# Kernel optimization log

Hardware: AMD Instinct MI355X
Metric: run time of the kernel (lower is better)

The kernel has to match this reference:

```python
import jax, jax.numpy as jnp
import numpy as np

NUM_BINS = 4
SCALE = 5.0
EPS = 1e-12

def hswish(x):
    return x * jnp.clip(x + 3.0, 0.0, 6.0) / 6.0

def l2norm(x, axis):
    n = jnp.sqrt(jnp.sum(x * x, axis=axis, keepdims=True))
    return x / jnp.maximum(n, EPS)

def setup_inputs() -> dict:
    key = jax.random.key(0)
    k0, k1, k2, k3, k4 = jax.random.split(key, 5)
    B, C, T, H, W = 8, 256, 32, 28, 28
    hidden, embd = 512, 32
    x = jax.random.normal(k0, (B, C, T, H, W), dtype=jnp.float32)
    W1 = jax.random.normal(k1, (hidden, C), dtype=jnp.float32) * (1.0 / np.sqrt(C))
    b1 = jax.random.normal(k2, (hidden,), dtype=jnp.float32) * 0.01
    W2 = jax.random.normal(k3, (embd, hidden), dtype=jnp.float32) * (1.0 / np.sqrt(hidden))
    b2 = jax.random.normal(k4, (embd,), dtype=jnp.float32) * 0.01
    return {"x": x, "W1": W1, "b1": b1, "W2": W2, "b2": b2}

def reference(x, W1, b1, W2, b2):
    B, C, T, H, W = x.shape
    # encoder: global spatial avg-pool -> 1x1x1 conv -> HSwish -> 1x1x1 conv
    pooled = jnp.mean(x, axis=(3, 4))                      # (B,C,T)
    h = hswish(jnp.einsum('hc,bct->bht', W1, pooled) + b1[None, :, None])
    embds = jnp.einsum('eh,bht->bet', W2, h) + b2[None, :, None]   # (B,E,T)
    norm_embd = l2norm(embds, axis=1)

    # --- grouping (no-grad in original) ---
    ns = jnp.sum(norm_embd[:, :, 1:] * norm_embd[:, :, :-1], axis=1)    # (B,T-1)
    # k-th smallest neighbour similarity = threshold
    smallest = -jax.lax.top_k(-ns, NUM_BINS - 1)[0]                      # ascending smallest k
    threshold = smallest[:, -1]
    edges = (ns > threshold[:, None]).astype(jnp.int32)                  # (B,T-1)
    interval_ends = jnp.concatenate(
        [jnp.zeros((B, 1), dtype=jnp.int32), 1 - edges], axis=1)        # (B,T)
    groups = jnp.cumsum(interval_ends, axis=1)                           # (B,T)
    group_ids = jnp.arange(NUM_BINS, dtype=groups.dtype)
    group_mask = (groups[:, :, None] == group_ids[None, None, :]).astype(jnp.float32)  # (B,T,K)
    group_sizes = jnp.sum(group_mask, axis=1, keepdims=True)             # (B,1,K)
    centers_sum = jnp.einsum('bet,btk->bek', norm_embd, group_mask)      # (B,E,K)
    norm_centers = l2norm(centers_sum / group_sizes, axis=1)             # (B,E,K)
    norm_centers = jax.lax.stop_gradient(norm_centers)

    similarities = jnp.einsum('bet,bek->btk', norm_embd, norm_centers)   # (B,T,K)
    weights = jax.nn.softmax(SCALE * similarities, axis=2)               # (B,T,K)
    sum_weights = jnp.sum(weights, axis=1, keepdims=True)                # (B,1,K)
    scales = jnp.where(sum_weights > 0.0, 1.0 / sum_weights, jnp.ones_like(sum_weights))
    scales = jax.lax.stop_gradient(scales)
    norm_weights = scales * weights                                      # (B,T,K)

    # weighted temporal pooling: avoids (B,C,T,K,H,W) blowup
    out = jnp.einsum('bcthw,btk->bckhw', x, norm_weights)                # (B,C,K,H,W)
    return out
```

## Files before the change

### kernel.cpp

```cpp
#include <hip/hip_runtime.h>
#include <math.h>

#define BATCH 8
#define CCH   256
#define TT    32
#define HWSZ  784
#define HID   512
#define EMB   32
#define KBINS 4
#define SCALEF 5.0f
#define EPSN  1e-12f

__global__ void pool_kernel(const float* __restrict__ x, float* __restrict__ pooled) {
    const int wave = threadIdx.x >> 6;
    const int lane = threadIdx.x & 63;
    const int row  = blockIdx.x * 4 + wave;
    const float4* xp = (const float4*)(x + (size_t)row * HWSZ);
    float s = 0.f;
    for (int f = lane; f < 196; f += 64) {
        float4 v = xp[f];
        s += v.x + v.y + v.z + v.w;
    }
#pragma unroll
    for (int off = 32; off > 0; off >>= 1) s += __shfl_down(s, off);
    if (lane == 0) pooled[row] = s * (1.0f / 784.0f);
}

__global__ void fc1_kernel(const float* __restrict__ W1, const float* __restrict__ b1,
                           const float* __restrict__ pooled, float* __restrict__ h) {
    const int b   = blockIdx.x >> 6;
    const int seg = blockIdx.x & 63;
    const int t   = threadIdx.x & 31;
    const int hid = seg * 8 + (threadIdx.x >> 5);
    const float* pb = pooled + (size_t)b * CCH * TT + t;
    const float* w  = W1 + (size_t)hid * CCH;
    float acc = 0.f;
#pragma unroll 8
    for (int c = 0; c < CCH; c++) acc += w[c] * pb[c * TT];
    acc += b1[hid];
    float r = fminf(fmaxf(acc + 3.0f, 0.0f), 6.0f);
    h[((size_t)b * HID + hid) * TT + t] = acc * r * (1.0f / 6.0f);
}

__global__ void fc2_kernel(const float* __restrict__ W2, const float* __restrict__ b2,
                           const float* __restrict__ h, float* __restrict__ embds) {
    const int o = blockIdx.x * 256 + threadIdx.x;
    const int b = o >> 10;
    const int e = (o >> 5) & 31;
    const int t = o & 31;
    const float* w  = W2 + (size_t)e * HID;
    const float* hp = h + (size_t)b * HID * TT + t;
    float acc = 0.f;
#pragma unroll 8
    for (int hd = 0; hd < HID; hd++) acc += w[hd] * hp[hd * TT];
    embds[o] = acc + b2[e];
}

__global__ void group_kernel(const float* __restrict__ embds, float* __restrict__ nw) {
    __shared__ float se[EMB][TT + 1];
    __shared__ float ns[TT];
    __shared__ float tmpns[TT];
    __shared__ float colinv[TT];
    __shared__ float cs[EMB][KBINS];
    __shared__ float wts[TT][KBINS];
    __shared__ float gsize[KBINS];
    __shared__ float kfac[KBINS];
    __shared__ int   gid[TT];

    const int b   = blockIdx.x;
    const int tid = threadIdx.x;

    for (int i = tid; i < EMB * TT; i += 256) {
        se[i >> 5][i & 31] = embds[(size_t)b * EMB * TT + i];
    }
    __syncthreads();

    if (tid < TT) {
        float s = 0.f;
        for (int e = 0; e < EMB; e++) { float v = se[e][tid]; s += v * v; }
        colinv[tid] = 1.0f / fmaxf(sqrtf(s), EPSN);
    }
    __syncthreads();
    for (int i = tid; i < EMB * TT; i += 256) {
        int e = i >> 5, t = i & 31;
        se[e][t] *= colinv[t];
    }
    __syncthreads();

    if (tid < TT - 1) {
        float s = 0.f;
        for (int e = 0; e < EMB; e++) s += se[e][tid] * se[e][tid + 1];
        ns[tid] = s;
    }
    __syncthreads();

    if (tid == 0) {
        for (int i = 0; i < TT - 1; i++) tmpns[i] = ns[i];
        float thr = 0.f;
        for (int p = 0; p < KBINS - 1; p++) {
            int jm = 0; float m = tmpns[0];
            for (int i = 1; i < TT - 1; i++) if (tmpns[i] < m) { m = tmpns[i]; jm = i; }
            thr = m;
            tmpns[jm] = __builtin_inff();
        }
        int g = 0; gid[0] = 0;
        for (int t = 1; t < TT; t++) { if (!(ns[t - 1] > thr)) g++; gid[t] = g; }
        for (int k = 0; k < KBINS; k++) {
            float c = 0.f;
            for (int t = 0; t < TT; t++) if (gid[t] == k) c += 1.0f;
            gsize[k] = c;
        }
    }
    __syncthreads();

    if (tid < EMB * KBINS) {
        int e = tid >> 2, k = tid & 3;
        float s = 0.f;
        for (int t = 0; t < TT; t++) if (gid[t] == k) s += se[e][t];
        cs[e][k] = s / gsize[k];
    }
    __syncthreads();
    if (tid < KBINS) {
        float s = 0.f;
        for (int e = 0; e < EMB; e++) { float v = cs[e][tid]; s += v * v; }
        kfac[tid] = 1.0f / fmaxf(sqrtf(s), EPSN);
    }
    __syncthreads();
    if (tid < EMB * KBINS) {
        int e = tid >> 2, k = tid & 3;
        cs[e][k] *= kfac[k];
    }
    __syncthreads();

    if (tid < TT * KBINS) {
        int t = tid >> 2, k = tid & 3;
        float s = 0.f;
        for (int e = 0; e < EMB; e++) s += se[e][t] * cs[e][k];
        wts[t][k] = s * SCALEF;
    }
    __syncthreads();
    if (tid < TT) {
        float m = wts[tid][0];
        for (int k = 1; k < KBINS; k++) m = fmaxf(m, wts[tid][k]);
        float ex[KBINS]; float sum = 0.f;
        for (int k = 0; k < KBINS; k++) { ex[k] = expf(wts[tid][k] - m); sum += ex[k]; }
        float inv = 1.0f / sum;
        for (int k = 0; k < KBINS; k++) wts[tid][k] = ex[k] * inv;
    }
    __syncthreads();
    if (tid < KBINS) {
        float s = 0.f;
        for (int t = 0; t < TT; t++) s += wts[t][tid];
        kfac[tid] = (s > 0.f) ? (1.0f / s) : 1.0f;
    }
    __syncthreads();
    if (tid < TT * KBINS) {
        int t = tid >> 2, k = tid & 3;
        nw[((size_t)b * TT + t) * KBINS + k] = wts[t][k] * kfac[k];
    }
}

__global__ void out_kernel(const float* __restrict__ x, const float* __restrict__ nw,
                           float* __restrict__ out) {
    __shared__ float w[TT * KBINS];
    const int b = blockIdx.x >> 8;
    const int c = blockIdx.x & 255;
    if (threadIdx.x < TT * KBINS) w[threadIdx.x] = nw[(size_t)b * TT * KBINS + threadIdx.x];
    __syncthreads();
    const int f = threadIdx.x;
    if (f >= 196) return;
    const float4* xp = (const float4*)(x + ((size_t)(b * CCH + c) * TT) * HWSZ);
    float4 acc[KBINS];
#pragma unroll
    for (int k = 0; k < KBINS; k++) { acc[k].x = 0.f; acc[k].y = 0.f; acc[k].z = 0.f; acc[k].w = 0.f; }
#pragma unroll 8
    for (int t = 0; t < TT; t++) {
        float4 v = xp[t * 196 + f];
#pragma unroll
        for (int k = 0; k < KBINS; k++) {
            float wk = w[t * KBINS + k];
            acc[k].x += v.x * wk;
            acc[k].y += v.y * wk;
            acc[k].z += v.z * wk;
            acc[k].w += v.w * wk;
        }
    }
    float4* op = (float4*)(out + ((size_t)(b * CCH + c) * KBINS) * HWSZ);
#pragma unroll
    for (int k = 0; k < KBINS; k++) op[k * 196 + f] = acc[k];
}

extern "C" void kernel_launch(void* const* d_in, const int* in_sizes, int n_in,
                              void* d_out, int out_size, void* d_ws, size_t ws_size,
                              hipStream_t stream) {
    const float* x  = (const float*)d_in[0];
    const float* W1 = (const float*)d_in[1];
    const float* b1 = (const float*)d_in[2];
    const float* W2 = (const float*)d_in[3];
    const float* b2 = (const float*)d_in[4];
    float* out = (float*)d_out;

    float* ws     = (float*)d_ws;
    float* pooled = ws;
    float* h      = pooled + BATCH * CCH * TT;
    float* embds  = h + BATCH * HID * TT;
    float* nw     = embds + BATCH * EMB * TT;

    pool_kernel<<<BATCH * CCH * TT / 4, 256, 0, stream>>>(x, pooled);
    fc1_kernel<<<BATCH * 64, 256, 0, stream>>>(W1, b1, pooled, h);
    fc2_kernel<<<BATCH * EMB * TT / 256, 256, 0, stream>>>(W2, b2, h, embds);
    group_kernel<<<BATCH, 256, 0, stream>>>(embds, nw);
    out_kernel<<<BATCH * CCH, 256, 0, stream>>>(x, nw, out);
}
```

Baseline: 360.8 us.

## Fuse pooling and MLP into one kernel and repack out_kernel threads

The separate pool, fc1 and fc2 kernels are merged into one 1024-thread kernel per (batch, time) column. It pools the spatial data into shared memory, then runs both fully connected layers from shared memory, which removes two launches and the global round trips for the intermediate tensors. The output kernel is also reorganised so every thread of a 256-thread block does work, instead of only 196 of 256. That cuts the block count, but it adds div/mod indexing and makes some blocks span two channels. The fused kernel has only 256 blocks for the pooling pass over x, which could limit memory-level parallelism.

```diff
diff --git a/kernel.cpp b/kernel.cpp
--- a/kernel.cpp
+++ b/kernel.cpp
@@ -11,49 +11,62 @@
 #define SCALEF 5.0f
 #define EPSN  1e-12f
 
-__global__ void pool_kernel(const float* __restrict__ x, float* __restrict__ pooled) {
-    const int wave = threadIdx.x >> 6;
-    const int lane = threadIdx.x & 63;
-    const int row  = blockIdx.x * 4 + wave;
-    const float4* xp = (const float4*)(x + (size_t)row * HWSZ);
-    float s = 0.f;
-    for (int f = lane; f < 196; f += 64) {
-        float4 v = xp[f];
-        s += v.x + v.y + v.z + v.w;
-    }
-#pragma unroll
-    for (int off = 32; off > 0; off >>= 1) s += __shfl_down(s, off);
-    if (lane == 0) pooled[row] = s * (1.0f / 784.0f);
-}
-
-__global__ void fc1_kernel(const float* __restrict__ W1, const float* __restrict__ b1,
-                           const float* __restrict__ pooled, float* __restrict__ h) {
-    const int b   = blockIdx.x >> 6;
-    const int seg = blockIdx.x & 63;
-    const int t   = threadIdx.x & 31;
-    const int hid = seg * 8 + (threadIdx.x >> 5);
-    const float* pb = pooled + (size_t)b * CCH * TT + t;
-    const float* w  = W1 + (size_t)hid * CCH;
-    float acc = 0.f;
+__global__ __launch_bounds__(1024) void mlp_kernel(
+        const float* __restrict__ x,
+        const float* __restrict__ W1, const float* __restrict__ b1,
+        const float* __restrict__ W2, const float* __restrict__ b2,
+        float* __restrict__ embds) {
+    __shared__ float pcol[CCH];
+    __shared__ float hcol[HID];
+
+    const int b = blockIdx.x >> 5;
+    const int t = blockIdx.x & 31;
+    const int tid  = threadIdx.x;
+    const int wave = tid >> 6;
+    const int lane = tid & 63;
+
+    for (int c = wave; c < CCH; c += 16) {
+        const float4* xp = (const float4*)(x + ((size_t)((b * CCH + c) * TT + t)) * HWSZ);
+        float s = 0.f;
+        for (int f = lane; f < 196; f += 64) {
+            float4 v = xp[f];
+            s += v.x + v.y + v.z + v.w;
+        }
+#pragma unroll
+        for (int off = 32; off > 0; off >>= 1) s += __shfl_down(s, off);
+        if (lane == 0) pcol[c] = s * (1.0f / 784.0f);
+    }
+    __syncthreads();
+
+    if (tid < HID) {
+        const float4* w = (const float4*)(W1 + (size_t)tid * CCH);
+        float acc = 0.f;
 #pragma unroll 8
-    for (int c = 0; c < CCH; c++) acc += w[c] * pb[c * TT];
-    acc += b1[hid];
-    float r = fminf(fmaxf(acc + 3.0f, 0.0f), 6.0f);
-    h[((size_t)b * HID + hid) * TT + t] = acc * r * (1.0f / 6.0f);
-}
-
-__global__ void fc2_kernel(const float* __restrict__ W2, const float* __restrict__ b2,
-                           const float* __restrict__ h, float* __restrict__ embds) {
-    const int o = blockIdx.x * 256 + threadIdx.x;
-    const int b = o >> 10;
-    const int e = (o >> 5) & 31;
-    const int t = o & 31;
-    const float* w  = W2 + (size_t)e * HID;
-    const float* hp = h + (size_t)b * HID * TT + t;
-    float acc = 0.f;
-#pragma unroll 8
-    for (int hd = 0; hd < HID; hd++) acc += w[hd] * hp[hd * TT];
-    embds[o] = acc + b2[e];
+        for (int j = 0; j < CCH / 4; j++) {
+            float4 wv = w[j];
+            acc += wv.x * pcol[4 * j] + wv.y * pcol[4 * j + 1]
+                 + wv.z * pcol[4 * j + 2] + wv.w * pcol[4 * j + 3];
+        }
+        acc += b1[tid];
+        float r = fminf(fmaxf(acc + 3.0f, 0.0f), 6.0f);
+        hcol[tid] = acc * r * (1.0f / 6.0f);
+    }
+    __syncthreads();
+
+    {
+        const int e = tid >> 5;
+        const int l = tid & 31;
+        const float* w = W2 + (size_t)e * HID;
+        float acc = 0.f;
+#pragma unroll
+        for (int j = 0; j < HID / 32; j++) acc += w[l + 32 * j] * hcol[l + 32 * j];
+        acc += __shfl_down(acc, 16);
+        acc += __shfl_down(acc, 8);
+        acc += __shfl_down(acc, 4);
+        acc += __shfl_down(acc, 2);
+        acc += __shfl_down(acc, 1);
+        if (l == 0) embds[((size_t)b * EMB + e) * TT + t] = acc + b2[e];
+    }
 }
 
 __global__ void group_kernel(const float* __restrict__ embds, float* __restrict__ nw) {
@@ -70,9 +83,8 @@
     const int b   = blockIdx.x;
     const int tid = threadIdx.x;
 
-    for (int i = tid; i < EMB * TT; i += 256) {
+    for (int i = tid; i < EMB * TT; i += 256)
         se[i >> 5][i & 31] = embds[(size_t)b * EMB * TT + i];
-    }
     __syncthreads();
 
     if (tid < TT) {
@@ -163,12 +175,12 @@
 __global__ void out_kernel(const float* __restrict__ x, const float* __restrict__ nw,
                            float* __restrict__ out) {
     __shared__ float w[TT * KBINS];
-    const int b = blockIdx.x >> 8;
-    const int c = blockIdx.x & 255;
+    const int b = blockIdx.x / 196;
+    const unsigned idx = (blockIdx.x % 196) * 256 + threadIdx.x;
     if (threadIdx.x < TT * KBINS) w[threadIdx.x] = nw[(size_t)b * TT * KBINS + threadIdx.x];
     __syncthreads();
-    const int f = threadIdx.x;
-    if (f >= 196) return;
+    const unsigned c = idx / 196;
+    const unsigned f = idx % 196;
     const float4* xp = (const float4*)(x + ((size_t)(b * CCH + c) * TT) * HWSZ);
     float4 acc[KBINS];
 #pragma unroll
@@ -200,15 +212,11 @@
     const float* b2 = (const float*)d_in[4];
     float* out = (float*)d_out;
 
-    float* ws     = (float*)d_ws;
-    float* pooled = ws;
-    float* h      = pooled + BATCH * CCH * TT;
-    float* embds  = h + BATCH * HID * TT;
-    float* nw     = embds + BATCH * EMB * TT;
-
-    pool_kernel<<<BATCH * CCH * TT / 4, 256, 0, stream>>>(x, pooled);
-    fc1_kernel<<<BATCH * 64, 256, 0, stream>>>(W1, b1, pooled, h);
-    fc2_kernel<<<BATCH * EMB * TT / 256, 256, 0, stream>>>(W2, b2, h, embds);
+    float* ws    = (float*)d_ws;
+    float* embds = ws;
+    float* nw    = embds + BATCH * EMB * TT;
+
+    mlp_kernel<<<BATCH * TT, 1024, 0, stream>>>(x, W1, b1, W2, b2, embds);
     group_kernel<<<BATCH, 256, 0, stream>>>(embds, nw);
-    out_kernel<<<BATCH * CCH, 256, 0, stream>>>(x, nw, out);
-}
+    out_kernel<<<BATCH * 196, 256, 0, stream>>>(x, nw, out);
+}
```

New measurement: 346.9 us. 1.04x faster.
